# Performance work log

Hardware: AMD Instinct MI355X
Metric: run time of the kernel (lower is better)

Reference implementation:

```python
import jax, jax.numpy as jnp
import numpy as np

BN_EPS = 1e-5

def _bn_relu(x, gamma, beta, mean, var):
    # x: [B, N, C]; BatchNorm1d(N) in eval mode normalizes over dim=1 (N)
    inv = jax.lax.rsqrt(var + BN_EPS)
    scale = (gamma * inv)[None, :, None]
    shift = (beta - mean * gamma * inv)[None, :, None]
    return jax.nn.relu(x * scale + shift)

def _forward(x, q_gamma, q_beta, q_mean, q_var,
             k_gamma, k_beta, k_mean, k_var,
             v_gamma, v_beta, v_mean, v_var,
             Wq, Wk, Wv, Wp):
    B, C, H, W = x.shape
    N = H * W
    E = Wq.shape[0]
    xs = x.reshape(B, C, N).transpose(0, 2, 1)  # [B, N, C]
    # BN+ReLU over spatial axis, then Linear(N->E) on spatial axis per channel -> [B, E, C]
    q = jnp.einsum('bnc,en->bec', _bn_relu(xs, q_gamma, q_beta, q_mean, q_var), Wq)
    k = jnp.einsum('bnc,en->bec', _bn_relu(xs, k_gamma, k_beta, k_mean, k_var), Wk)
    v = jnp.einsum('bnc,en->bec', _bn_relu(xs, v_gamma, v_beta, v_mean, v_var), Wv)
    scores = jnp.einsum('bec,bfc->bef', q, k) / jnp.sqrt(jnp.asarray(E, x.dtype))  # [B, E, E]
    attn = jax.nn.softmax(scores, axis=-1)
    out = jnp.einsum('bef,bfc->bec', attn, v)          # [B, E, C]
    out = jnp.einsum('bec,ne->bcn', out, Wp)            # Linear(E->N) -> [B, C, N]
    return out.reshape(B, C, H, W)

def setup_inputs() -> dict:
    key = jax.random.key(0)
    ks = jax.random.split(key, 20)
    B, C, H, W = 32, 512, 32, 32
    N = H * W  # sp_dim = 1024
    E = 1024   # embed_dim
    d = {'x': jax.random.normal(ks[0], (B, C, H, W), jnp.float32)}
    i = 1
    for p in ('q', 'k', 'v'):
        d[f'{p}_gamma'] = jax.random.uniform(ks[i], (N,), jnp.float32, 0.5, 1.5); i += 1
        d[f'{p}_beta'] = 0.1 * jax.random.normal(ks[i], (N,), jnp.float32); i += 1
        d[f'{p}_mean'] = 0.1 * jax.random.normal(ks[i], (N,), jnp.float32); i += 1
        d[f'{p}_var'] = jax.random.uniform(ks[i], (N,), jnp.float32, 0.5, 1.5); i += 1
    # torch Linear weight layout: [out, in]; scale ~ 1/sqrt(fan_in)
    d['Wq'] = jax.random.normal(ks[i], (E, N), jnp.float32) * (1.0 / np.sqrt(N)); i += 1
    d['Wk'] = jax.random.normal(ks[i], (E, N), jnp.float32) * (1.0 / np.sqrt(N)); i += 1
    d['Wv'] = jax.random.normal(ks[i], (E, N), jnp.float32) * (1.0 / np.sqrt(N)); i += 1
    d['Wp'] = jax.random.normal(ks[i], (N, E), jnp.float32) * (1.0 / np.sqrt(E)); i += 1
    return d

def reference(x, q_gamma, q_beta, q_mean, q_var,
              k_gamma, k_beta, k_mean, k_var,
              v_gamma, v_beta, v_mean, v_var,
              Wq, Wk, Wv, Wp):
    return _forward(x, q_gamma, q_beta, q_mean, q_var,
                    k_gamma, k_beta, k_mean, k_var,
                    v_gamma, v_beta, v_mean, v_var,
                    Wq, Wk, Wv, Wp)
```

## Files before the change

kernel.cpp:

```cpp
#include <hip/hip_runtime.h>
#include <math.h>

#define BN_EPS 1e-5f

namespace {

constexpr int Bb = 32;
constexpr int Cc = 512;
constexpr int Nn = 1024;
constexpr int Ee = 1024;

typedef __attribute__((ext_vector_type(8))) short short8;
typedef __attribute__((ext_vector_type(4))) float f32x4;
typedef __attribute__((ext_vector_type(4))) unsigned short ushort4_t;

struct bfpair { unsigned short h, l; };

__device__ __forceinline__ unsigned short bf16_rne(float v) {
  unsigned u = __builtin_bit_cast(unsigned, v);
  unsigned r = u + 0x7FFFu + ((u >> 16) & 1u);
  return (unsigned short)(r >> 16);
}
__device__ __forceinline__ float bf16_to_f(unsigned short h) {
  unsigned u = ((unsigned)h) << 16;
  return __builtin_bit_cast(float, u);
}
__device__ __forceinline__ bfpair split_bf(float v) {
  bfpair p;
  p.h = bf16_rne(v);
  p.l = bf16_rne(v - bf16_to_f(p.h));
  return p;
}

__device__ __forceinline__ void gll16(const void* g, void* l) {
  __builtin_amdgcn_global_load_lds(
      (const __attribute__((address_space(1))) void*)g,
      (__attribute__((address_space(3))) void*)l, 16, 0, 0);
}

__global__ __launch_bounds__(256) void prep_st_kernel(
    const float* __restrict__ g, const float* __restrict__ be,
    const float* __restrict__ mn, const float* __restrict__ vr,
    float* __restrict__ s, float* __restrict__ t, int n) {
  int i = blockIdx.x * blockDim.x + threadIdx.x;
  if (i < n) {
    float inv = rsqrtf(vr[i] + BN_EPS);
    float sc = g[i] * inv;
    s[i] = sc;
    t[i] = be[i] - mn[i] * sc;
  }
}

__global__ __launch_bounds__(256) void convert_y(
    const float* __restrict__ x, const float* __restrict__ s, const float* __restrict__ tt,
    unsigned short* __restrict__ yh, unsigned short* __restrict__ yl, long total4) {
  for (long i = (long)blockIdx.x * 256 + threadIdx.x; i < total4; i += (long)gridDim.x * 256) {
    float4 v = ((const float4*)x)[i];
    int n4 = (int)(i & 255);
    float4 s4 = ((const float4*)s)[n4];
    float4 t4 = ((const float4*)tt)[n4];
    float e0 = fmaxf(fmaf(v.x, s4.x, t4.x), 0.f);
    float e1 = fmaxf(fmaf(v.y, s4.y, t4.y), 0.f);
    float e2 = fmaxf(fmaf(v.z, s4.z, t4.z), 0.f);
    float e3 = fmaxf(fmaf(v.w, s4.w, t4.w), 0.f);
    bfpair p0 = split_bf(e0), p1 = split_bf(e1), p2 = split_bf(e2), p3 = split_bf(e3);
    ushort4_t hv, lv;
    hv.x = p0.h; hv.y = p1.h; hv.z = p2.h; hv.w = p3.h;
    lv.x = p0.l; lv.y = p1.l; lv.z = p2.l; lv.w = p3.l;
    *(ushort4_t*)&yh[i * 4] = hv;
    *(ushort4_t*)&yl[i * 4] = lv;
  }
}

__global__ __launch_bounds__(256) void convert_w(
    const float* __restrict__ wsrc, unsigned short* __restrict__ wh,
    unsigned short* __restrict__ wl, long total4) {
  for (long i = (long)blockIdx.x * 256 + threadIdx.x; i < total4; i += (long)gridDim.x * 256) {
    float4 v = ((const float4*)wsrc)[i];
    bfpair p0 = split_bf(v.x), p1 = split_bf(v.y), p2 = split_bf(v.z), p3 = split_bf(v.w);
    ushort4_t hv, lv;
    hv.x = p0.h; hv.y = p1.h; hv.z = p2.h; hv.w = p3.h;
    lv.x = p0.l; lv.y = p1.l; lv.z = p2.l; lv.w = p3.l;
    *(ushort4_t*)&wh[i * 4] = hv;
    *(ushort4_t*)&wl[i * 4] = lv;
  }
}

template<bool SPLIT>
__global__ __launch_bounds__(256) void gemm3(
    const unsigned short* __restrict__ Ah, const unsigned short* __restrict__ Al,
    long ldA, long bsA,
    const unsigned short* __restrict__ Bh, const unsigned short* __restrict__ Bl,
    long ldB, long bsB,
    float* __restrict__ Cf, unsigned short* __restrict__ Chi, unsigned short* __restrict__ Clo,
    long ldC, long bsC, int K, float alpha) {
  __shared__ unsigned short sAh[128][32], sAl[128][32], sBh[128][32], sBl[128][32];

  const int t = threadIdx.x, lane = t & 63, w = t >> 6;
  const int m0 = blockIdx.y * 128, n0 = blockIdx.x * 128;
  const long zb = blockIdx.z;

  const int sr = lane >> 2;
  const int sk = (lane & 3) * 8;
  const int wr = w >> 1, wc = w & 1;
  const int fr = lane & 15;
  const int kq = (lane >> 4) * 8;

  const unsigned short* a0 = Ah + zb * bsA + (long)(m0 + w * 32 + sr) * ldA + sk;
  const unsigned short* a1 = Al + zb * bsA + (long)(m0 + w * 32 + sr) * ldA + sk;
  const unsigned short* b0 = Bh + zb * bsB + (long)(n0 + w * 32 + sr) * ldB + sk;
  const unsigned short* b1 = Bl + zb * bsB + (long)(n0 + w * 32 + sr) * ldB + sk;
  const long a16 = 16 * ldA, b16 = 16 * ldB;

  f32x4 acc[4][4] = {};

  for (int k0 = 0; k0 < K; k0 += 32) {
    __syncthreads();
    gll16(a0, &sAh[w * 32][0]);      gll16(a0 + a16, &sAh[w * 32 + 16][0]);
    gll16(a1, &sAl[w * 32][0]);      gll16(a1 + a16, &sAl[w * 32 + 16][0]);
    gll16(b0, &sBh[w * 32][0]);      gll16(b0 + b16, &sBh[w * 32 + 16][0]);
    gll16(b1, &sBl[w * 32][0]);      gll16(b1 + b16, &sBl[w * 32 + 16][0]);
    a0 += 32; a1 += 32; b0 += 32; b1 += 32;
    __syncthreads();

    short8 ah[4], al[4], bh[4], bl[4];
#pragma unroll
    for (int i = 0; i < 4; ++i) {
      ah[i] = *(const short8*)&sAh[wr * 64 + i * 16 + fr][kq];
      al[i] = *(const short8*)&sAl[wr * 64 + i * 16 + fr][kq];
      bh[i] = *(const short8*)&sBh[wc * 64 + i * 16 + fr][kq];
      bl[i] = *(const short8*)&sBl[wc * 64 + i * 16 + fr][kq];
    }
#pragma unroll
    for (int i = 0; i < 4; ++i)
#pragma unroll
      for (int j = 0; j < 4; ++j) {
        acc[i][j] = __builtin_amdgcn_mfma_f32_16x16x32_bf16(ah[i], bh[j], acc[i][j], 0, 0, 0);
        acc[i][j] = __builtin_amdgcn_mfma_f32_16x16x32_bf16(ah[i], bl[j], acc[i][j], 0, 0, 0);
        acc[i][j] = __builtin_amdgcn_mfma_f32_16x16x32_bf16(al[i], bh[j], acc[i][j], 0, 0, 0);
      }
  }

  const int rb = (lane >> 4) * 4;
#pragma unroll
  for (int i = 0; i < 4; ++i)
#pragma unroll
    for (int j = 0; j < 4; ++j) {
      long col = n0 + wc * 64 + j * 16 + fr;
#pragma unroll
      for (int v = 0; v < 4; ++v) {
        long row = m0 + wr * 64 + i * 16 + rb + v;
        float val = acc[i][j][v] * alpha;
        long idx = zb * bsC + row * ldC + col;
        if (SPLIT) {
          bfpair p = split_bf(val);
          Chi[idx] = p.h;
          Clo[idx] = p.l;
        } else {
          Cf[idx] = val;
        }
      }
    }
}

__global__ __launch_bounds__(256) void softmax_rows(float* __restrict__ S) {
  long row = blockIdx.x;
  float* p = S + row * 1024;
  int t = threadIdx.x;
  float4 v = *(float4*)(p + 4 * t);
  float mx = fmaxf(fmaxf(v.x, v.y), fmaxf(v.z, v.w));
#pragma unroll
  for (int i = 1; i < 64; i <<= 1) mx = fmaxf(mx, __shfl_xor(mx, i));
  __shared__ float redm[4];
  __shared__ float reds[4];
  int wave = t >> 6, lane = t & 63;
  if (lane == 0) redm[wave] = mx;
  __syncthreads();
  mx = fmaxf(fmaxf(redm[0], redm[1]), fmaxf(redm[2], redm[3]));
  float e0 = expf(v.x - mx), e1 = expf(v.y - mx);
  float e2 = expf(v.z - mx), e3 = expf(v.w - mx);
  float sum = (e0 + e1) + (e2 + e3);
#pragma unroll
  for (int i = 1; i < 64; i <<= 1) sum += __shfl_xor(sum, i);
  if (lane == 0) reds[wave] = sum;
  __syncthreads();
  sum = (reds[0] + reds[1]) + (reds[2] + reds[3]);
  float inv = 1.0f / sum;
  bfpair p0 = split_bf(e0 * inv), p1 = split_bf(e1 * inv);
  bfpair p2 = split_bf(e2 * inv), p3 = split_bf(e3 * inv);
  ushort4_t hv, lv;
  hv.x = p0.h; hv.y = p1.h; hv.z = p2.h; hv.w = p3.h;
  lv.x = p0.l; lv.y = p1.l; lv.z = p2.l; lv.w = p3.l;
  unsigned short* ph = (unsigned short*)p;
  *(ushort4_t*)&ph[4 * t] = hv;
  *(ushort4_t*)&ph[1024 + 4 * t] = lv;
}

}

extern "C" void kernel_launch(void* const* d_in, const int* in_sizes, int n_in,
                              void* d_out, int out_size, void* d_ws, size_t ws_size,
                              hipStream_t stream) {
  const float* x  = (const float*)d_in[0];
  const float* qg = (const float*)d_in[1];
  const float* qb = (const float*)d_in[2];
  const float* qm = (const float*)d_in[3];
  const float* qv = (const float*)d_in[4];
  const float* kg = (const float*)d_in[5];
  const float* kb = (const float*)d_in[6];
  const float* km = (const float*)d_in[7];
  const float* kv = (const float*)d_in[8];
  const float* vg = (const float*)d_in[9];
  const float* vb = (const float*)d_in[10];
  const float* vm = (const float*)d_in[11];
  const float* vv = (const float*)d_in[12];
  const float* Wq = (const float*)d_in[13];
  const float* Wk = (const float*)d_in[14];
  const float* Wv = (const float*)d_in[15];
  const float* Wp = (const float*)d_in[16];

  const size_t wMB = 8UL * 1024 * 1024 * 2;
  const size_t perB = 12UL * 1024 * 1024;
  int G = 32;
  while (G > 1 && 65536 + wMB + (size_t)G * perB > ws_size) G >>= 1;

  char* ws = (char*)d_ws;
  float* sq = (float*)ws;
  float* tq = sq + 1024;
  float* sk = tq + 1024;
  float* tk = sk + 1024;
  float* sv = tk + 1024;
  float* tv = sv + 1024;

  const long WE = 1024L * 1024;
  unsigned short* Wqh = (unsigned short*)(ws + 65536);
  unsigned short* Wql = Wqh + WE;
  unsigned short* Wkh = Wql + WE;
  unsigned short* Wkl = Wkh + WE;
  unsigned short* Wvh = Wkl + WE;
  unsigned short* Wvl = Wvh + WE;
  unsigned short* Wph = Wvl + WE;
  unsigned short* Wpl = Wph + WE;

  const long PB = (long)Cc * Ee;
  unsigned short* yh  = Wpl + WE;
  unsigned short* yl  = yh + (long)G * PB;
  unsigned short* Qh  = yl + (long)G * PB;
  unsigned short* Ql  = Qh + (long)G * PB;
  unsigned short* Kh  = Ql + (long)G * PB;
  unsigned short* Kl  = Kh + (long)G * PB;
  unsigned short* Vth = Kl + (long)G * PB;
  unsigned short* Vtl = Vth + (long)G * PB;
  float* S = (float*)(Vtl + (long)G * PB);
  unsigned short* Oth = Qh;
  unsigned short* Otl = Ql;

  dim3 blk(256);

  prep_st_kernel<<<dim3(4), blk, 0, stream>>>(qg, qb, qm, qv, sq, tq, Nn);
  prep_st_kernel<<<dim3(4), blk, 0, stream>>>(kg, kb, km, kv, sk, tk, Nn);
  prep_st_kernel<<<dim3(4), blk, 0, stream>>>(vg, vb, vm, vv, sv, tv, Nn);

  const long W4 = WE / 4;
  convert_w<<<dim3(1024), blk, 0, stream>>>(Wq, Wqh, Wql, W4);
  convert_w<<<dim3(1024), blk, 0, stream>>>(Wk, Wkh, Wkl, W4);
  convert_w<<<dim3(1024), blk, 0, stream>>>(Wv, Wvh, Wvl, W4);
  convert_w<<<dim3(1024), blk, 0, stream>>>(Wp, Wph, Wpl, W4);

  const long y4 = (long)G * PB / 4;

  for (int b0 = 0; b0 < Bb; b0 += G) {
    const float* xg = x + (size_t)b0 * Cc * Nn;
    float* outg = (float*)d_out + (size_t)b0 * Cc * Nn;

    convert_y<<<dim3(2048), blk, 0, stream>>>(xg, sq, tq, yh, yl, y4);
    gemm3<true><<<dim3(Cc / 128, Ee / 128, G), blk, 0, stream>>>(
        Wqh, Wql, Nn, 0L, yh, yl, Nn, PB,
        nullptr, Qh, Ql, Cc, PB, Nn, 1.0f);
    convert_y<<<dim3(2048), blk, 0, stream>>>(xg, sk, tk, yh, yl, y4);
    gemm3<true><<<dim3(Cc / 128, Ee / 128, G), blk, 0, stream>>>(
        Wkh, Wkl, Nn, 0L, yh, yl, Nn, PB,
        nullptr, Kh, Kl, Cc, PB, Nn, 1.0f);
    convert_y<<<dim3(2048), blk, 0, stream>>>(xg, sv, tv, yh, yl, y4);
    gemm3<true><<<dim3(Ee / 128, Cc / 128, G), blk, 0, stream>>>(
        yh, yl, Nn, PB, Wvh, Wvl, Nn, 0L,
        nullptr, Vth, Vtl, Ee, PB, Nn, 1.0f);
    gemm3<false><<<dim3(Ee / 128, Ee / 128, G), blk, 0, stream>>>(
        Qh, Ql, Cc, PB, Kh, Kl, Cc, PB,
        S, nullptr, nullptr, Ee, (long)Ee * Ee, Cc, 0.03125f);
    softmax_rows<<<dim3(G * Ee), blk, 0, stream>>>(S);
    gemm3<true><<<dim3(Ee / 128, Cc / 128, G), blk, 0, stream>>>(
        Vth, Vtl, Ee, PB, (unsigned short*)S, (unsigned short*)S + 1024,
        2L * Ee, 2L * Ee * Ee,
        nullptr, Oth, Otl, Ee, PB, Ee, 1.0f);
    gemm3<false><<<dim3(Nn / 128, Cc / 128, G), blk, 0, stream>>>(
        Oth, Otl, Ee, PB, Wph, Wpl, Ee, 0L,
        outg, nullptr, nullptr, Nn, (long)Cc * Nn, Ee, 1.0f);
  }
}
```

Baseline: 865.5 us.

## Fuse BN conversions, swizzle LDS layout, and remap GEMM blocks for XCD locality

The three BN+ReLU bf16-split conversions are merged into one kernel, so x is read once and written to separate Q/K/V input buffers. The GEMM now uses an XOR swizzle on the LDS k-offset for both the global-to-LDS copy and the fragment reads, meant to cut LDS bank conflicts. It also switches to a 1D grid whose block index is remapped across the 8 XCDs, so neighbouring tiles share L2. The larger workspace per batch may lower the batch group size G when workspace is tight.

After: 1.196 ms. 38.2% more time.

```diff
diff --git a/kernel.cpp b/kernel.cpp
--- a/kernel.cpp
+++ b/kernel.cpp
@@ -51,24 +51,50 @@
   }
 }
 
-__global__ __launch_bounds__(256) void convert_y(
-    const float* __restrict__ x, const float* __restrict__ s, const float* __restrict__ tt,
-    unsigned short* __restrict__ yh, unsigned short* __restrict__ yl, long total4) {
+__global__ __launch_bounds__(256) void convert_y3(
+    const float* __restrict__ x,
+    const float* __restrict__ sq, const float* __restrict__ tq,
+    const float* __restrict__ sk, const float* __restrict__ tk,
+    const float* __restrict__ sv, const float* __restrict__ tv,
+    unsigned short* __restrict__ yqh, unsigned short* __restrict__ yql,
+    unsigned short* __restrict__ ykh, unsigned short* __restrict__ ykl,
+    unsigned short* __restrict__ yvh, unsigned short* __restrict__ yvl,
+    long total4) {
   for (long i = (long)blockIdx.x * 256 + threadIdx.x; i < total4; i += (long)gridDim.x * 256) {
     float4 v = ((const float4*)x)[i];
     int n4 = (int)(i & 255);
-    float4 s4 = ((const float4*)s)[n4];
-    float4 t4 = ((const float4*)tt)[n4];
-    float e0 = fmaxf(fmaf(v.x, s4.x, t4.x), 0.f);
-    float e1 = fmaxf(fmaf(v.y, s4.y, t4.y), 0.f);
-    float e2 = fmaxf(fmaf(v.z, s4.z, t4.z), 0.f);
-    float e3 = fmaxf(fmaf(v.w, s4.w, t4.w), 0.f);
-    bfpair p0 = split_bf(e0), p1 = split_bf(e1), p2 = split_bf(e2), p3 = split_bf(e3);
+    float4 a, b;
     ushort4_t hv, lv;
-    hv.x = p0.h; hv.y = p1.h; hv.z = p2.h; hv.w = p3.h;
-    lv.x = p0.l; lv.y = p1.l; lv.z = p2.l; lv.w = p3.l;
-    *(ushort4_t*)&yh[i * 4] = hv;
-    *(ushort4_t*)&yl[i * 4] = lv;
+    a = ((const float4*)sq)[n4]; b = ((const float4*)tq)[n4];
+    {
+      bfpair p0 = split_bf(fmaxf(fmaf(v.x, a.x, b.x), 0.f));
+      bfpair p1 = split_bf(fmaxf(fmaf(v.y, a.y, b.y), 0.f));
+      bfpair p2 = split_bf(fmaxf(fmaf(v.z, a.z, b.z), 0.f));
+      bfpair p3 = split_bf(fmaxf(fmaf(v.w, a.w, b.w), 0.f));
+      hv.x = p0.h; hv.y = p1.h; hv.z = p2.h; hv.w = p3.h;
+      lv.x = p0.l; lv.y = p1.l; lv.z = p2.l; lv.w = p3.l;
+      *(ushort4_t*)&yqh[i * 4] = hv; *(ushort4_t*)&yql[i * 4] = lv;
+    }
+    a = ((const float4*)sk)[n4]; b = ((const float4*)tk)[n4];
+    {
+      bfpair p0 = split_bf(fmaxf(fmaf(v.x, a.x, b.x), 0.f));
+      bfpair p1 = split_bf(fmaxf(fmaf(v.y, a.y, b.y), 0.f));
+      bfpair p2 = split_bf(fmaxf(fmaf(v.z, a.z, b.z), 0.f));
+      bfpair p3 = split_bf(fmaxf(fmaf(v.w, a.w, b.w), 0.f));
+      hv.x = p0.h; hv.y = p1.h; hv.z = p2.h; hv.w = p3.h;
+      lv.x = p0.l; lv.y = p1.l; lv.z = p2.l; lv.w = p3.l;
+      *(ushort4_t*)&ykh[i * 4] = hv; *(ushort4_t*)&ykl[i * 4] = lv;
+    }
+    a = ((const float4*)sv)[n4]; b = ((const float4*)tv)[n4];
+    {
+      bfpair p0 = split_bf(fmaxf(fmaf(v.x, a.x, b.x), 0.f));
+      bfpair p1 = split_bf(fmaxf(fmaf(v.y, a.y, b.y), 0.f));
+      bfpair p2 = split_bf(fmaxf(fmaf(v.z, a.z, b.z), 0.f));
+      bfpair p3 = split_bf(fmaxf(fmaf(v.w, a.w, b.w), 0.f));
+      hv.x = p0.h; hv.y = p1.h; hv.z = p2.h; hv.w = p3.h;
+      lv.x = p0.l; lv.y = p1.l; lv.z = p2.l; lv.w = p3.l;
+      *(ushort4_t*)&yvh[i * 4] = hv; *(ushort4_t*)&yvl[i * 4] = lv;
+    }
   }
 }
 
@@ -93,18 +119,23 @@
     const unsigned short* __restrict__ Bh, const unsigned short* __restrict__ Bl,
     long ldB, long bsB,
     float* __restrict__ Cf, unsigned short* __restrict__ Chi, unsigned short* __restrict__ Clo,
-    long ldC, long bsC, int K, float alpha) {
+    long ldC, long bsC, int K, float alpha, int gx, int gy) {
   __shared__ unsigned short sAh[128][32], sAl[128][32], sBh[128][32], sBl[128][32];
 
+  const int nb = gridDim.x;
+  int f = blockIdx.x;
+  if ((nb & 7) == 0) f = (f & 7) * (nb >> 3) + (f >> 3);
+  const int n0 = (f % gx) * 128;
+  const int m0 = ((f / gx) % gy) * 128;
+  const long zb = f / (gx * gy);
+
   const int t = threadIdx.x, lane = t & 63, w = t >> 6;
-  const int m0 = blockIdx.y * 128, n0 = blockIdx.x * 128;
-  const long zb = blockIdx.z;
 
   const int sr = lane >> 2;
-  const int sk = (lane & 3) * 8;
+  const int sk = (((lane & 3) ^ ((lane >> 3) & 3)) * 8);
   const int wr = w >> 1, wc = w & 1;
   const int fr = lane & 15;
-  const int kq = (lane >> 4) * 8;
+  const int kq = ((((lane >> 4) & 3) ^ ((fr >> 1) & 3)) * 8);
 
   const unsigned short* a0 = Ah + zb * bsA + (long)(m0 + w * 32 + sr) * ldA + sk;
   const unsigned short* a1 = Al + zb * bsA + (long)(m0 + w * 32 + sr) * ldA + sk;
@@ -141,7 +172,7 @@
       }
   }
 
-  const int rb = (lane >> 4) * 4;
+  const int rb = ((lane >> 4) & 3) * 4;
 #pragma unroll
   for (int i = 0; i < 4; ++i)
 #pragma unroll
@@ -219,8 +250,8 @@
   const float* Wv = (const float*)d_in[15];
   const float* Wp = (const float*)d_in[16];
 
-  const size_t wMB = 8UL * 1024 * 1024 * 2;
-  const size_t perB = 12UL * 1024 * 1024;
+  const size_t wMB  = 16UL * 1024 * 1024;
+  const size_t perB = 16UL * 1024 * 1024;
   int G = 32;
   while (G > 1 && 65536 + wMB + (size_t)G * perB > ws_size) G >>= 1;
 
@@ -243,9 +274,13 @@
   unsigned short* Wpl = Wph + WE;
 
   const long PB = (long)Cc * Ee;
-  unsigned short* yh  = Wpl + WE;
-  unsigned short* yl  = yh + (long)G * PB;
-  unsigned short* Qh  = yl + (long)G * PB;
+  unsigned short* yqh = Wpl + WE;
+  unsigned short* yql = yqh + (long)G * PB;
+  unsigned short* ykh = yql + (long)G * PB;
+  unsigned short* ykl = ykh + (long)G * PB;
+  unsigned short* yvh = ykl + (long)G * PB;
+  unsigned short* yvl = yvh + (long)G * PB;
+  unsigned short* Qh  = yvl + (long)G * PB;
   unsigned short* Ql  = Qh + (long)G * PB;
   unsigned short* Kh  = Ql + (long)G * PB;
   unsigned short* Kl  = Kh + (long)G * PB;
@@ -273,28 +308,28 @@
     const float* xg = x + (size_t)b0 * Cc * Nn;
     float* outg = (float*)d_out + (size_t)b0 * Cc * Nn;
 
-    convert_y<<<dim3(2048), blk, 0, stream>>>(xg, sq, tq, yh, yl, y4);
-    gemm3<true><<<dim3(Cc / 128, Ee / 128, G), blk, 0, stream>>>(
-        Wqh, Wql, Nn, 0L, yh, yl, Nn, PB,
-        nullptr, Qh, Ql, Cc, PB, Nn, 1.0f);
-    convert_y<<<dim3(2048), blk, 0, stream>>>(xg, sk, tk, yh, yl, y4);
-    gemm3<true><<<dim3(Cc / 128, Ee / 128, G), blk, 0, stream>>>(
-        Wkh, Wkl, Nn, 0L, yh, yl, Nn, PB,
-        nullptr, Kh, Kl, Cc, PB, Nn, 1.0f);
-    convert_y<<<dim3(2048), blk, 0, stream>>>(xg, sv, tv, yh, yl, y4);
-    gemm3<true><<<dim3(Ee / 128, Cc / 128, G), blk, 0, stream>>>(
-        yh, yl, Nn, PB, Wvh, Wvl, Nn, 0L,
-        nullptr, Vth, Vtl, Ee, PB, Nn, 1.0f);
-    gemm3<false><<<dim3(Ee / 128, Ee / 128, G), blk, 0, stream>>>(
+    convert_y3<<<dim3(2048), blk, 0, stream>>>(
+        xg, sq, tq, sk, tk, sv, tv, yqh, yql, ykh, ykl, yvh, yvl, y4);
+
+    gemm3<true><<<dim3((Cc / 128) * (Ee / 128) * G), blk, 0, stream>>>(
+        Wqh, Wql, Nn, 0L, yqh, yql, Nn, PB,
+        nullptr, Qh, Ql, Cc, PB, Nn, 1.0f, Cc / 128, Ee / 128);
+    gemm3<true><<<dim3((Cc / 128) * (Ee / 128) * G), blk, 0, stream>>>(
+        Wkh, Wkl, Nn, 0L, ykh, ykl, Nn, PB,
+        nullptr, Kh, Kl, Cc, PB, Nn, 1.0f, Cc / 128, Ee / 128);
+    gemm3<true><<<dim3((Ee / 128) * (Cc / 128) * G), blk, 0, stream>>>(
+        yvh, yvl, Nn, PB, Wvh, Wvl, Nn, 0L,
+        nullptr, Vth, Vtl, Ee, PB, Nn, 1.0f, Ee / 128, Cc / 128);
+    gemm3<false><<<dim3((Ee / 128) * (Ee / 128) * G), blk, 0, stream>>>(
         Qh, Ql, Cc, PB, Kh, Kl, Cc, PB,
-        S, nullptr, nullptr, Ee, (long)Ee * Ee, Cc, 0.03125f);
+        S, nullptr, nullptr, Ee, (long)Ee * Ee, Cc, 0.03125f, Ee / 128, Ee / 128);
     softmax_rows<<<dim3(G * Ee), blk, 0, stream>>>(S);
-    gemm3<true><<<dim3(Ee / 128, Cc / 128, G), blk, 0, stream>>>(
+    gemm3<true><<<dim3((Ee / 128) * (Cc / 128) * G), blk, 0, stream>>>(
         Vth, Vtl, Ee, PB, (unsigned short*)S, (unsigned short*)S + 1024,
         2L * Ee, 2L * Ee * Ee,
-        nullptr, Oth, Otl, Ee, PB, Ee, 1.0f);
-    gemm3<false><<<dim3(Nn / 128, Cc / 128, G), blk, 0, stream>>>(
+        nullptr, Oth, Otl, Ee, PB, Ee, 1.0f, Ee / 128, Cc / 128);
+    gemm3<false><<<dim3((Nn / 128) * (Cc / 128) * G), blk, 0, stream>>>(
         Oth, Otl, Ee, PB, Wph, Wpl, Ee, 0L,
-        outg, nullptr, nullptr, Nn, (long)Cc * Nn, Ee, 1.0f);
-  }
-}
+        outg, nullptr, nullptr, Nn, (long)Cc * Nn, Ee, 1.0f, Nn / 128, Cc / 128);
+  }
+}
```
